# Kernel optimization log

Measured on AMD Instinct MI355X. Metric: run time of the kernel, lower is better.

Reference implementation:

```python
import jax, jax.numpy as jnp
import numpy as np


def _lstm_layer(x, Wih, Whh, bih, bhh):
    """Single-layer LSTM, batch_first, zero init state. PyTorch gate order i,f,g,o.
    x: [B,T,F]; Wih: [4H,F]; Whh: [4H,H]; bih,bhh: [4H]. Returns (outputs [B,T,H], h_T [B,H])."""
    B = x.shape[0]
    H = Whh.shape[1]
    # Precompute input projection for all timesteps (one big GEMM).
    pre = jnp.einsum('btf,gf->btg', x, Wih) + (bih + bhh)  # [B,T,4H]
    pre = jnp.swapaxes(pre, 0, 1)  # time-major [T,B,4H]

    def step(carry, p):
        h, c = carry
        gates = p + h @ Whh.T  # [B,4H]
        i, f, g, o = jnp.split(gates, 4, axis=-1)
        i = jax.nn.sigmoid(i)
        f = jax.nn.sigmoid(f)
        g = jnp.tanh(g)
        o = jax.nn.sigmoid(o)
        c = f * c + i * g
        h = o * jnp.tanh(c)
        return (h, c), h

    h0 = jnp.zeros((B, H), x.dtype)
    (hT, cT), hs = jax.lax.scan(step, (h0, h0), pre)
    return jnp.swapaxes(hs, 0, 1), hT


def setup_inputs() -> dict:
    key = jax.random.key(0)
    ks = jax.random.split(key, 20)
    B, T, F = 4096, 200, 36
    H1, H2, H3 = 16, 32, 16
    NC = 6

    def u(k, shape, h):
        s = 1.0 / np.sqrt(h)
        return jax.random.uniform(k, shape, jnp.float32, -s, s)

    inp = {
        'x': jax.random.normal(ks[0], (B, T, F), jnp.float32),
        'Wih1': u(ks[1], (4 * H1, F), H1), 'Whh1': u(ks[2], (4 * H1, H1), H1),
        'bih1': u(ks[3], (4 * H1,), H1), 'bhh1': u(ks[4], (4 * H1,), H1),
        'Wih2': u(ks[5], (4 * H2, H1), H2), 'Whh2': u(ks[6], (4 * H2, H2), H2),
        'bih2': u(ks[7], (4 * H2,), H2), 'bhh2': u(ks[8], (4 * H2,), H2),
        'Wih3': u(ks[9], (4 * H3, H2), H3), 'Whh3': u(ks[10], (4 * H3, H3), H3),
        'bih3': u(ks[11], (4 * H3,), H3), 'bhh3': u(ks[12], (4 * H3,), H3),
        'W_fc1': u(ks[13], (128, H3), H3), 'b_fc1': u(ks[14], (128,), H3),
        'W_fc2': u(ks[15], (32, 128), 128), 'b_fc2': u(ks[16], (32,), 128),
        'W_cls': u(ks[17], (NC, 32), 32), 'b_cls': u(ks[18], (NC,), 32),
    }
    return inp


def reference(x, Wih1, Whh1, bih1, bhh1, Wih2, Whh2, bih2, bhh2,
              Wih3, Whh3, bih3, bhh3, W_fc1, b_fc1, W_fc2, b_fc2, W_cls, b_cls):
    out1, _ = _lstm_layer(x, Wih1, Whh1, bih1, bhh1)
    out2, _ = _lstm_layer(out1, Wih2, Whh2, bih2, bhh2)
    _, hn = _lstm_layer(out2, Wih3, Whh3, bih3, bhh3)  # final hidden state [B,16]
    out = hn @ W_fc1.T + b_fc1
    out = out @ W_fc2.T + b_fc2
    out = out @ W_cls.T + b_cls
    return out
```

## Files before the change

kernel.cpp:

```cpp
#include <hip/hip_runtime.h>

typedef _Float16 hv8 __attribute__((ext_vector_type(8)));
typedef float    fv4 __attribute__((ext_vector_type(4)));
typedef unsigned int u32;

#define DEVI __device__ __forceinline__

static constexpr int T_   = 200;
static constexpr int ROWS = 8;
static constexpr int WS   = 72;
static constexpr int BTOT = 4096;

static constexpr int F1o = 0;
static constexpr int F2o = 1024;
static constexpr int XAo = 3072;
static constexpr int XBo = 3584;
static constexpr int F3o = 4096;
static constexpr int F_TOTAL = 4608;

#if __has_builtin(__builtin_amdgcn_rcpf)
DEVI float frcp(float x) { return __builtin_amdgcn_rcpf(x); }
#else
DEVI float frcp(float x) { return 1.0f / x; }
#endif
DEVI float fsig(float x)  { return frcp(1.0f + __expf(-x)); }
DEVI float ftanh(float x) { float e = __expf(2.0f * x); return 1.0f - 2.0f * frcp(e + 1.0f); }

DEVI u32 pk2h(float a, float b) {
    union { _Float16 h[2]; u32 u; } cv;
    cv.h[0] = (_Float16)a; cv.h[1] = (_Float16)b;
    return cv.u;
}

union HU { hv8 h; u32 u[4]; };

__global__ __launch_bounds__(256, 2) void lstm_fused(
    const float* __restrict__ xg,
    const float* __restrict__ Wih1, const float* __restrict__ Whh1,
    const float* __restrict__ bih1, const float* __restrict__ bhh1,
    const float* __restrict__ Wih2, const float* __restrict__ Whh2,
    const float* __restrict__ bih2, const float* __restrict__ bhh2,
    const float* __restrict__ Wih3, const float* __restrict__ Whh3,
    const float* __restrict__ bih3, const float* __restrict__ bhh3,
    const float* __restrict__ W_fc1, const float* __restrict__ b_fc1,
    const float* __restrict__ W_fc2, const float* __restrict__ b_fc2,
    const float* __restrict__ W_cls, const float* __restrict__ b_cls,
    float* __restrict__ outp)
{
    __shared__ __align__(16) _Float16 poolH[256 * WS];
    __shared__ float T2s[512];
    __shared__ float t2vs[32];
    __shared__ float Msh[96];
    __shared__ float vsh[6];

    const int tid  = threadIdx.x;
    const int wid  = tid >> 6;
    const int lane = tid & 63;
    const int nl   = lane & 15;
    const int quad = lane >> 4;
    const int b0   = blockIdx.x * ROWS;

    for (int idx = tid; idx < 256 * WS; idx += 256) {
        int n = idx / WS, k = idx - n * WS;
        int w = n >> 6, r = n & 63;
        int g = r >> 4, u = r & 15;
        float v = 0.f;
        if (w == 0) {
            int row = g * 16 + u;
            if (k < 36)       v = Wih1[row * 36 + k];
            else if (k == 36) v = bih1[row] + bhh1[row];
            else if (k >= 48 && k < 64) v = Whh1[row * 16 + (k - 48)];
        } else if (w <= 2) {
            int row = g * 32 + (w - 1) * 16 + u;
            if (k < 16)       v = Wih2[row * 16 + k];
            else if (k < 48)  {
                int kk = k - 16;
                int uu = (w == 1) ? kk : ((kk < 16) ? kk + 16 : kk - 16);
                v = Whh2[row * 32 + uu];
            }
            else if (k == 48) v = bih2[row] + bhh2[row];
        } else {
            int row = g * 16 + u;
            if (k < 32)       v = Wih3[row * 32 + k];
            else if (k < 48)  v = Whh3[row * 16 + (k - 32)];
            else if (k == 48) v = bih3[row] + bhh3[row];
        }
        poolH[idx] = (_Float16)v;
    }
    for (int idx = tid; idx < 512; idx += 256) {
        int b = idx >> 4, u = idx & 15;
        float acc = 0.f;
        for (int a = 0; a < 128; ++a) acc += W_fc2[b * 128 + a] * W_fc1[a * 16 + u];
        T2s[idx] = acc;
    }
    if (tid < 32) {
        float acc = b_fc2[tid];
        for (int a = 0; a < 128; ++a) acc += W_fc2[tid * 128 + a] * b_fc1[a];
        t2vs[tid] = acc;
    }
    __syncthreads();

    hv8 Wf[2][4];
    #pragma unroll
    for (int kt = 0; kt < 2; ++kt)
        #pragma unroll
        for (int mt = 0; mt < 4; ++mt)
            Wf[kt][mt] = *(const hv8*)&poolH[(wid * 64 + mt * 16 + nl) * WS + kt * 32 + quad * 8];
    if (tid < 96) {
        int u = tid / 6, j = tid - (tid / 6) * 6;
        float acc = 0.f;
        for (int b = 0; b < 32; ++b) acc += W_cls[j * 32 + b] * T2s[b * 16 + u];
        Msh[u * 6 + j] = acc;
    }
    if (tid < 6) {
        float acc = b_cls[tid];
        for (int b = 0; b < 32; ++b) acc += W_cls[tid * 32 + b] * t2vs[b];
        vsh[tid] = acc;
    }
    __syncthreads();

    for (int idx = tid; idx < F_TOTAL; idx += 256) poolH[idx] = (_Float16)0.f;

    fv4 xc[2][3], xn[2][3];
    const float* xb = xg;
    if (wid == 0) {
        int xr = b0 + nl; if (xr > BTOT - 1) xr = BTOT - 1;
        xb = xg + (size_t)xr * T_ * 36;
        #pragma unroll
        for (int g = 0; g < 2; ++g) {
            xn[g][0] = *(const fv4*)(xb + g * 36 + quad * 8);
            xn[g][1] = *(const fv4*)(xb + g * 36 + quad * 8 + 4);
            xn[g][2] = *(const fv4*)(xb + g * 36 + 32);
        }
    }
    __syncthreads();

    u32 pk01 = 0, pk23 = 0;
    float c_st[4] = {0.f, 0.f, 0.f, 0.f};
    const int s1x4 = ((quad & 1) * 32 + nl) * 4;
    const int s2x4 = s1x4 + 64;
    const u32 BIAS1 = 0x00003C00u;

    const int NI = T_ / 2 + 2;
    for (int s = 0; s < NI; ++s) {
        const int pp = (s - 1) & 1, wp = s & 1;
        bool act;
        if (wid == 0)      act = (s < T_ / 2);
        else if (wid <= 2) act = (s >= 1 && s <= T_ / 2);
        else               act = (s >= 2);

        HU pf0, pf1, pfx;
        if (act) {
            if (wid == 0) {
                #pragma unroll
                for (int g = 0; g < 2; ++g) { xc[g][0]=xn[g][0]; xc[g][1]=xn[g][1]; xc[g][2]=xn[g][2]; }
                #pragma unroll
                for (int g = 0; g < 2; ++g) {
                    int t = 2 * s + 2 + g;
                    if (t < T_) {
                        xn[g][0] = *(const fv4*)(xb + t * 36 + quad * 8);
                        xn[g][1] = *(const fv4*)(xb + t * 36 + quad * 8 + 4);
                        xn[g][2] = *(const fv4*)(xb + t * 36 + 32);
                    }
                }
            } else if (wid <= 2) {
                pf0.h = *(const hv8*)&poolH[F1o + ((pp * 2 + 0) * 16 + nl) * 16 + (quad & 1) * 8];
                pf1.h = *(const hv8*)&poolH[F1o + ((pp * 2 + 1) * 16 + nl) * 16 + (quad & 1) * 8];
                const int sibX = (wid == 1) ? XBo : XAo;
                pfx.h = *(const hv8*)&poolH[sibX + (1 * 16 + nl) * 16 + (quad & 1) * 8];
            } else {
                pf0.h = *(const hv8*)&poolH[F2o + ((pp * 2 + 0) * 16 + nl) * 32 + quad * 8];
                pf1.h = *(const hv8*)&poolH[F2o + ((pp * 2 + 1) * 16 + nl) * 32 + quad * 8];
            }

            HU x2g1;
            #pragma unroll
            for (int g = 0; g < 2; ++g) {
                u32 sA = (u32)__builtin_amdgcn_ds_bpermute(s1x4, (int)pk01);
                u32 sB = (u32)__builtin_amdgcn_ds_bpermute(s1x4, (int)pk23);
                u32 sC = (u32)__builtin_amdgcn_ds_bpermute(s2x4, (int)pk01);
                u32 sD = (u32)__builtin_amdgcn_ds_bpermute(s2x4, (int)pk23);

                HU bk0, bk1;
                if (wid == 0) {
                    bk0.u[0] = pk2h(xc[g][0][0], xc[g][0][1]);
                    bk0.u[1] = pk2h(xc[g][0][2], xc[g][0][3]);
                    bk0.u[2] = pk2h(xc[g][1][0], xc[g][1][1]);
                    bk0.u[3] = pk2h(xc[g][1][2], xc[g][1][3]);
                    if (quad >= 2) { bk1.u[0]=sA; bk1.u[1]=sB; bk1.u[2]=sC; bk1.u[3]=sD; }
                    else {
                        bk1.u[0] = pk2h(xc[g][2][0], xc[g][2][1]);
                        bk1.u[1] = pk2h(xc[g][2][2], xc[g][2][3]);
                        bk1.u[2] = BIAS1; bk1.u[3] = 0u;
                    }
                } else if (wid <= 2) {
                    if (quad < 2) bk0 = g ? pf1 : pf0;
                    else { bk0.u[0]=sA; bk0.u[1]=sB; bk0.u[2]=sC; bk0.u[3]=sD; }
                    if (quad < 2) bk1 = g ? x2g1 : pfx;
                    else { bk1.u[0]=BIAS1; bk1.u[1]=0u; bk1.u[2]=0u; bk1.u[3]=0u; }
                } else {
                    bk0 = g ? pf1 : pf0;
                    if (quad < 2) { bk1.u[0]=sA; bk1.u[1]=sB; bk1.u[2]=sC; bk1.u[3]=sD; }
                    else { bk1.u[0]=BIAS1; bk1.u[1]=0u; bk1.u[2]=0u; bk1.u[3]=0u; }
                }

                fv4 C[4] = {(fv4){0,0,0,0}, (fv4){0,0,0,0}, (fv4){0,0,0,0}, (fv4){0,0,0,0}};
                #pragma unroll
                for (int mt = 0; mt < 4; ++mt) C[mt] = __builtin_amdgcn_mfma_f32_16x16x32_f16(Wf[0][mt], bk0.h, C[mt], 0, 0, 0);
                #pragma unroll
                for (int mt = 0; mt < 4; ++mt) C[mt] = __builtin_amdgcn_mfma_f32_16x16x32_f16(Wf[1][mt], bk1.h, C[mt], 0, 0, 0);

                float h4[4];
                #pragma unroll
                for (int r = 0; r < 4; ++r) {
                    float gi = fsig(C[0][r]);
                    float gf = fsig(C[1][r]);
                    float gg = ftanh(C[2][r]);
                    float go = fsig(C[3][r]);
                    float c  = gf * c_st[r] + gi * gg;
                    c_st[r] = c;
                    h4[r] = go * ftanh(c);
                }
                pk01 = pk2h(h4[0], h4[1]);
                pk23 = pk2h(h4[2], h4[3]);

                if (wid == 0) {
                    u32* f1 = (u32*)&poolH[F1o + ((wp * 2 + g) * 16 + nl) * 16 + quad * 4];
                    f1[0] = pk01; f1[1] = pk23;
                } else if (wid <= 2) {
                    const int ownX = (wid == 1) ? XAo : XBo;
                    u32* xo = (u32*)&poolH[ownX + (g * 16 + nl) * 16 + quad * 4];
                    xo[0] = pk01; xo[1] = pk23;
                    const int ub = (wid == 1) ? 0 : 16;
                    u32* f2 = (u32*)&poolH[F2o + ((wp * 2 + g) * 16 + nl) * 32 + ub + quad * 4];
                    f2[0] = pk01; f2[1] = pk23;
                    if (g == 0) {
                        const int sibX = (wid == 1) ? XBo : XAo;
                        x2g1.h = *(const hv8*)&poolH[sibX + (0 * 16 + nl) * 16 + (quad & 1) * 8];
                    }
                } else {
                    u32* f3 = (u32*)&poolH[F3o + (g * 16 + nl) * 16 + quad * 4];
                    f3[0] = pk01; f3[1] = pk23;
                }
            }
        }
        __syncthreads();
    }

    if (tid < ROWS * 6) {
        int row = tid / 6, j = tid - (tid / 6) * 6;
        float acc = vsh[j];
        const int hb = F3o + 16 * 16 + row * 16;
        #pragma unroll
        for (int u = 0; u < 16; ++u)
            acc += (float)poolH[hb + u] * Msh[u * 6 + j];
        outp[(b0 + row) * 6 + j] = acc;
    }
}

extern "C" void kernel_launch(void* const* d_in, const int* in_sizes, int n_in,
                              void* d_out, int out_size, void* d_ws, size_t ws_size,
                              hipStream_t stream) {
    const float* x     = (const float*)d_in[0];
    const float* Wih1  = (const float*)d_in[1];
    const float* Whh1  = (const float*)d_in[2];
    const float* bih1  = (const float*)d_in[3];
    const float* bhh1  = (const float*)d_in[4];
    const float* Wih2  = (const float*)d_in[5];
    const float* Whh2  = (const float*)d_in[6];
    const float* bih2  = (const float*)d_in[7];
    const float* bhh2  = (const float*)d_in[8];
    const float* Wih3  = (const float*)d_in[9];
    const float* Whh3  = (const float*)d_in[10];
    const float* bih3  = (const float*)d_in[11];
    const float* bhh3  = (const float*)d_in[12];
    const float* W_fc1 = (const float*)d_in[13];
    const float* b_fc1 = (const float*)d_in[14];
    const float* W_fc2 = (const float*)d_in[15];
    const float* b_fc2 = (const float*)d_in[16];
    const float* W_cls = (const float*)d_in[17];
    const float* b_cls = (const float*)d_in[18];

    lstm_fused<<<512, 256, 0, stream>>>(x,
        Wih1, Whh1, bih1, bhh1,
        Wih2, Whh2, bih2, bhh2,
        Wih3, Whh3, bih3, bhh3,
        W_fc1, b_fc1, W_fc2, b_fc2, W_cls, b_cls,
        (float*)d_out);
}
```

Baseline: 435.9 us.

## Split recurrent MFMA from input projection to shorten per-step dependency chain

Reorganises the weight layout so each wave keeps separate input-projection and recurrent weight fragments. The input-side MFMAs for both sub-steps of an iteration are issued up front, off the recurrent critical path, and only one recurrent MFMA per gate tile remains serialised behind the bpermute of the previous hidden state. It also prefetches x two iterations ahead and replaces __syncthreads with a raw waitcnt+s_barrier. This costs extra MFMAs for layer 1 and more weight registers, and the hand-written barrier depends on LDS ordering being correct.

```diff
diff --git a/kernel.cpp b/kernel.cpp
--- a/kernel.cpp
+++ b/kernel.cpp
@@ -8,7 +8,7 @@
 
 static constexpr int T_   = 200;
 static constexpr int ROWS = 8;
-static constexpr int WS   = 72;
+static constexpr int WS   = 104;
 static constexpr int BTOT = 4096;
 
 static constexpr int F1o = 0;
@@ -69,21 +69,21 @@
             int row = g * 16 + u;
             if (k < 36)       v = Wih1[row * 36 + k];
             else if (k == 36) v = bih1[row] + bhh1[row];
-            else if (k >= 48 && k < 64) v = Whh1[row * 16 + (k - 48)];
+            else if (k >= 64 && k < 80) v = Whh1[row * 16 + (k - 64)];
         } else if (w <= 2) {
             int row = g * 32 + (w - 1) * 16 + u;
             if (k < 16)       v = Wih2[row * 16 + k];
-            else if (k < 48)  {
-                int kk = k - 16;
+            else if (k == 16) v = bih2[row] + bhh2[row];
+            else if (k >= 64 && k < 96) {
+                int kk = k - 64;
                 int uu = (w == 1) ? kk : ((kk < 16) ? kk + 16 : kk - 16);
                 v = Whh2[row * 32 + uu];
             }
-            else if (k == 48) v = bih2[row] + bhh2[row];
         } else {
             int row = g * 16 + u;
             if (k < 32)       v = Wih3[row * 32 + k];
-            else if (k < 48)  v = Whh3[row * 16 + (k - 32)];
-            else if (k == 48) v = bih3[row] + bhh3[row];
+            else if (k >= 64 && k < 80) v = Whh3[row * 16 + (k - 64)];
+            else if (k == 80) v = bih3[row] + bhh3[row];
         }
         poolH[idx] = (_Float16)v;
     }
@@ -100,12 +100,18 @@
     }
     __syncthreads();
 
-    hv8 Wf[2][4];
+    hv8 WI0[4], WI1[4], WH[4];
     #pragma unroll
-    for (int kt = 0; kt < 2; ++kt)
+    for (int mt = 0; mt < 4; ++mt) {
+        const int base = (wid * 64 + mt * 16 + nl) * WS;
+        WI0[mt] = *(const hv8*)&poolH[base + quad * 8];
+        WH[mt]  = *(const hv8*)&poolH[base + 64 + quad * 8];
+    }
+    if (wid == 0) {
         #pragma unroll
         for (int mt = 0; mt < 4; ++mt)
-            Wf[kt][mt] = *(const hv8*)&poolH[(wid * 64 + mt * 16 + nl) * WS + kt * 32 + quad * 8];
+            WI1[mt] = *(const hv8*)&poolH[(mt * 16 + nl) * WS + 32 + quad * 8];
+    }
     if (tid < 96) {
         int u = tid / 6, j = tid - (tid / 6) * 6;
         float acc = 0.f;
@@ -128,9 +134,12 @@
         xb = xg + (size_t)xr * T_ * 36;
         #pragma unroll
         for (int g = 0; g < 2; ++g) {
-            xn[g][0] = *(const fv4*)(xb + g * 36 + quad * 8);
-            xn[g][1] = *(const fv4*)(xb + g * 36 + quad * 8 + 4);
-            xn[g][2] = *(const fv4*)(xb + g * 36 + 32);
+            xc[g][0] = *(const fv4*)(xb + g * 36 + quad * 8);
+            xc[g][1] = *(const fv4*)(xb + g * 36 + quad * 8 + 4);
+            xc[g][2] = *(const fv4*)(xb + g * 36 + 32);
+            xn[g][0] = *(const fv4*)(xb + (2 + g) * 36 + quad * 8);
+            xn[g][1] = *(const fv4*)(xb + (2 + g) * 36 + quad * 8 + 4);
+            xn[g][2] = *(const fv4*)(xb + (2 + g) * 36 + 32);
         }
     }
     __syncthreads();
@@ -140,6 +149,54 @@
     const int s1x4 = ((quad & 1) * 32 + nl) * 4;
     const int s2x4 = s1x4 + 64;
     const u32 BIAS1 = 0x00003C00u;
+    const fv4 Z4 = (fv4){0.f, 0.f, 0.f, 0.f};
+
+#define DO_STEP(CARR, G)                                                              \
+    {                                                                                 \
+        u32 sA = (u32)__builtin_amdgcn_ds_bpermute(s1x4, (int)pk01);                  \
+        u32 sB = (u32)__builtin_amdgcn_ds_bpermute(s1x4, (int)pk23);                  \
+        u32 sC = (u32)__builtin_amdgcn_ds_bpermute(s2x4, (int)pk01);                  \
+        u32 sD = (u32)__builtin_amdgcn_ds_bpermute(s2x4, (int)pk23);                  \
+        HU bh;                                                                        \
+        if (quad < 2) { bh.u[0]=sA; bh.u[1]=sB; bh.u[2]=sC; bh.u[3]=sD; }             \
+        else if (wid == 0) { bh.u[0]=0u; bh.u[1]=0u; bh.u[2]=0u; bh.u[3]=0u; }        \
+        else if (wid <= 2) { bh = (G) ? x2g1 : pfx; }                                 \
+        else { bh.u[0]=(quad==2)?BIAS1:0u; bh.u[1]=0u; bh.u[2]=0u; bh.u[3]=0u; }      \
+        _Pragma("unroll")                                                             \
+        for (int mt = 0; mt < 4; ++mt)                                                \
+            CARR[mt] = __builtin_amdgcn_mfma_f32_16x16x32_f16(WH[mt], bh.h, CARR[mt], 0, 0, 0); \
+        float h4[4];                                                                  \
+        _Pragma("unroll")                                                             \
+        for (int r = 0; r < 4; ++r) {                                                 \
+            float gi = fsig(CARR[0][r]);                                              \
+            float gf = fsig(CARR[1][r]);                                              \
+            float gg = ftanh(CARR[2][r]);                                             \
+            float go = fsig(CARR[3][r]);                                              \
+            float c  = gf * c_st[r] + gi * gg;                                        \
+            c_st[r] = c;                                                              \
+            h4[r] = go * ftanh(c);                                                    \
+        }                                                                             \
+        pk01 = pk2h(h4[0], h4[1]);                                                    \
+        pk23 = pk2h(h4[2], h4[3]);                                                    \
+        if (wid == 0) {                                                               \
+            u32* f1 = (u32*)&poolH[F1o + ((wp * 2 + (G)) * 16 + nl) * 16 + quad * 4]; \
+            f1[0] = pk01; f1[1] = pk23;                                               \
+        } else if (wid <= 2) {                                                        \
+            const int ownX = (wid == 1) ? XAo : XBo;                                  \
+            u32* xo = (u32*)&poolH[ownX + ((G) * 16 + nl) * 16 + quad * 4];           \
+            xo[0] = pk01; xo[1] = pk23;                                               \
+            const int ub = (wid == 1) ? 0 : 16;                                       \
+            u32* f2 = (u32*)&poolH[F2o + ((wp * 2 + (G)) * 16 + nl) * 32 + ub + quad * 4]; \
+            f2[0] = pk01; f2[1] = pk23;                                               \
+            if ((G) == 0) {                                                           \
+                const int sibX = (wid == 1) ? XBo : XAo;                              \
+                x2g1.h = *(const hv8*)&poolH[sibX + (0 * 16 + nl) * 16 + (quad & 1) * 8]; \
+            }                                                                         \
+        } else {                                                                      \
+            u32* f3 = (u32*)&poolH[F3o + ((G) * 16 + nl) * 16 + quad * 4];            \
+            f3[0] = pk01; f3[1] = pk23;                                               \
+        }                                                                             \
+    }
 
     const int NI = T_ / 2 + 2;
     for (int s = 0; s < NI; ++s) {
@@ -149,14 +206,36 @@
         else if (wid <= 2) act = (s >= 1 && s <= T_ / 2);
         else               act = (s >= 2);
 
-        HU pf0, pf1, pfx;
         if (act) {
+            fv4 C0[4] = {Z4, Z4, Z4, Z4};
+            fv4 C1[4] = {Z4, Z4, Z4, Z4};
+            HU pfx, x2g1;
+
             if (wid == 0) {
                 #pragma unroll
+                for (int g = 0; g < 2; ++g) {
+                    HU bx0, bx1;
+                    bx0.u[0] = pk2h(xc[g][0][0], xc[g][0][1]);
+                    bx0.u[1] = pk2h(xc[g][0][2], xc[g][0][3]);
+                    bx0.u[2] = pk2h(xc[g][1][0], xc[g][1][1]);
+                    bx0.u[3] = pk2h(xc[g][1][2], xc[g][1][3]);
+                    if (quad == 0) {
+                        bx1.u[0] = pk2h(xc[g][2][0], xc[g][2][1]);
+                        bx1.u[1] = pk2h(xc[g][2][2], xc[g][2][3]);
+                        bx1.u[2] = BIAS1; bx1.u[3] = 0u;
+                    } else { bx1.u[0]=0u; bx1.u[1]=0u; bx1.u[2]=0u; bx1.u[3]=0u; }
+                    #pragma unroll
+                    for (int mt = 0; mt < 4; ++mt) {
+                        fv4* Cg = g ? C1 : C0;
+                        Cg[mt] = __builtin_amdgcn_mfma_f32_16x16x32_f16(WI0[mt], bx0.h, Cg[mt], 0, 0, 0);
+                        Cg[mt] = __builtin_amdgcn_mfma_f32_16x16x32_f16(WI1[mt], bx1.h, Cg[mt], 0, 0, 0);
+                    }
+                }
+                #pragma unroll
                 for (int g = 0; g < 2; ++g) { xc[g][0]=xn[g][0]; xc[g][1]=xn[g][1]; xc[g][2]=xn[g][2]; }
                 #pragma unroll
                 for (int g = 0; g < 2; ++g) {
-                    int t = 2 * s + 2 + g;
+                    int t = 2 * s + 4 + g;
                     if (t < T_) {
                         xn[g][0] = *(const fv4*)(xb + t * 36 + quad * 8);
                         xn[g][1] = *(const fv4*)(xb + t * 36 + quad * 8 + 4);
@@ -164,87 +243,37 @@
                     }
                 }
             } else if (wid <= 2) {
+                HU pf0, pf1;
                 pf0.h = *(const hv8*)&poolH[F1o + ((pp * 2 + 0) * 16 + nl) * 16 + (quad & 1) * 8];
                 pf1.h = *(const hv8*)&poolH[F1o + ((pp * 2 + 1) * 16 + nl) * 16 + (quad & 1) * 8];
-                const int sibX = (wid == 1) ? XBo : XAo;
-                pfx.h = *(const hv8*)&poolH[sibX + (1 * 16 + nl) * 16 + (quad & 1) * 8];
+                {
+                    const int sibX = (wid == 1) ? XBo : XAo;
+                    pfx.h = *(const hv8*)&poolH[sibX + (1 * 16 + nl) * 16 + (quad & 1) * 8];
+                }
+                HU b0, b1;
+                if (quad < 2)      { b0 = pf0; b1 = pf1; }
+                else if (quad == 2){ b0.u[0]=BIAS1; b0.u[1]=0u; b0.u[2]=0u; b0.u[3]=0u; b1 = b0; }
+                else               { b0.u[0]=0u; b0.u[1]=0u; b0.u[2]=0u; b0.u[3]=0u; b1 = b0; }
+                #pragma unroll
+                for (int mt = 0; mt < 4; ++mt) {
+                    C0[mt] = __builtin_amdgcn_mfma_f32_16x16x32_f16(WI0[mt], b0.h, C0[mt], 0, 0, 0);
+                    C1[mt] = __builtin_amdgcn_mfma_f32_16x16x32_f16(WI0[mt], b1.h, C1[mt], 0, 0, 0);
+                }
             } else {
-                pf0.h = *(const hv8*)&poolH[F2o + ((pp * 2 + 0) * 16 + nl) * 32 + quad * 8];
-                pf1.h = *(const hv8*)&poolH[F2o + ((pp * 2 + 1) * 16 + nl) * 32 + quad * 8];
+                HU b0, b1;
+                b0.h = *(const hv8*)&poolH[F2o + ((pp * 2 + 0) * 16 + nl) * 32 + quad * 8];
+                b1.h = *(const hv8*)&poolH[F2o + ((pp * 2 + 1) * 16 + nl) * 32 + quad * 8];
+                #pragma unroll
+                for (int mt = 0; mt < 4; ++mt) {
+                    C0[mt] = __builtin_amdgcn_mfma_f32_16x16x32_f16(WI0[mt], b0.h, C0[mt], 0, 0, 0);
+                    C1[mt] = __builtin_amdgcn_mfma_f32_16x16x32_f16(WI0[mt], b1.h, C1[mt], 0, 0, 0);
+                }
             }
 
-            HU x2g1;
-            #pragma unroll
-            for (int g = 0; g < 2; ++g) {
-                u32 sA = (u32)__builtin_amdgcn_ds_bpermute(s1x4, (int)pk01);
-                u32 sB = (u32)__builtin_amdgcn_ds_bpermute(s1x4, (int)pk23);
-                u32 sC = (u32)__builtin_amdgcn_ds_bpermute(s2x4, (int)pk01);
-                u32 sD = (u32)__builtin_amdgcn_ds_bpermute(s2x4, (int)pk23);
-
-                HU bk0, bk1;
-                if (wid == 0) {
-                    bk0.u[0] = pk2h(xc[g][0][0], xc[g][0][1]);
-                    bk0.u[1] = pk2h(xc[g][0][2], xc[g][0][3]);
-                    bk0.u[2] = pk2h(xc[g][1][0], xc[g][1][1]);
-                    bk0.u[3] = pk2h(xc[g][1][2], xc[g][1][3]);
-                    if (quad >= 2) { bk1.u[0]=sA; bk1.u[1]=sB; bk1.u[2]=sC; bk1.u[3]=sD; }
-                    else {
-                        bk1.u[0] = pk2h(xc[g][2][0], xc[g][2][1]);
-                        bk1.u[1] = pk2h(xc[g][2][2], xc[g][2][3]);
-                        bk1.u[2] = BIAS1; bk1.u[3] = 0u;
-                    }
-                } else if (wid <= 2) {
-                    if (quad < 2) bk0 = g ? pf1 : pf0;
-                    else { bk0.u[0]=sA; bk0.u[1]=sB; bk0.u[2]=sC; bk0.u[3]=sD; }
-                    if (quad < 2) bk1 = g ? x2g1 : pfx;
-                    else { bk1.u[0]=BIAS1; bk1.u[1]=0u; bk1.u[2]=0u; bk1.u[3]=0u; }
-                } else {
-                    bk0 = g ? pf1 : pf0;
-                    if (quad < 2) { bk1.u[0]=sA; bk1.u[1]=sB; bk1.u[2]=sC; bk1.u[3]=sD; }
-                    else { bk1.u[0]=BIAS1; bk1.u[1]=0u; bk1.u[2]=0u; bk1.u[3]=0u; }
-                }
-
-                fv4 C[4] = {(fv4){0,0,0,0}, (fv4){0,0,0,0}, (fv4){0,0,0,0}, (fv4){0,0,0,0}};
-                #pragma unroll
-                for (int mt = 0; mt < 4; ++mt) C[mt] = __builtin_amdgcn_mfma_f32_16x16x32_f16(Wf[0][mt], bk0.h, C[mt], 0, 0, 0);
-                #pragma unroll
-                for (int mt = 0; mt < 4; ++mt) C[mt] = __builtin_amdgcn_mfma_f32_16x16x32_f16(Wf[1][mt], bk1.h, C[mt], 0, 0, 0);
-
-                float h4[4];
-                #pragma unroll
-                for (int r = 0; r < 4; ++r) {
-                    float gi = fsig(C[0][r]);
-                    float gf = fsig(C[1][r]);
-                    float gg = ftanh(C[2][r]);
-                    float go = fsig(C[3][r]);
-                    float c  = gf * c_st[r] + gi * gg;
-                    c_st[r] = c;
-                    h4[r] = go * ftanh(c);
-                }
-                pk01 = pk2h(h4[0], h4[1]);
-                pk23 = pk2h(h4[2], h4[3]);
-
-                if (wid == 0) {
-                    u32* f1 = (u32*)&poolH[F1o + ((wp * 2 + g) * 16 + nl) * 16 + quad * 4];
-                    f1[0] = pk01; f1[1] = pk23;
-                } else if (wid <= 2) {
-                    const int ownX = (wid == 1) ? XAo : XBo;
-                    u32* xo = (u32*)&poolH[ownX + (g * 16 + nl) * 16 + quad * 4];
-                    xo[0] = pk01; xo[1] = pk23;
-                    const int ub = (wid == 1) ? 0 : 16;
-                    u32* f2 = (u32*)&poolH[F2o + ((wp * 2 + g) * 16 + nl) * 32 + ub + quad * 4];
-                    f2[0] = pk01; f2[1] = pk23;
-                    if (g == 0) {
-                        const int sibX = (wid == 1) ? XBo : XAo;
-                        x2g1.h = *(const hv8*)&poolH[sibX + (0 * 16 + nl) * 16 + (quad & 1) * 8];
-                    }
-                } else {
-                    u32* f3 = (u32*)&poolH[F3o + (g * 16 + nl) * 16 + quad * 4];
-                    f3[0] = pk01; f3[1] = pk23;
-                }
-            }
+            DO_STEP(C0, 0)
+            DO_STEP(C1, 1)
         }
-        __syncthreads();
+        asm volatile("s_waitcnt lgkmcnt(0)\n\ts_barrier" ::: "memory");
     }
 
     if (tid < ROWS * 6) {
@@ -256,6 +285,7 @@
             acc += (float)poolH[hb + u] * Msh[u * 6 + j];
         outp[(b0 + row) * 6 + j] = acc;
     }
+#undef DO_STEP
 }
 
 extern "C" void kernel_launch(void* const* d_in, const int* in_sizes, int n_in,
```

Result: slower. 449.3 us (+3.1%).

## Split LSTM cell activations across lanes using DPP rotate to halve transcendental work

Applied to the files above, without the earlier changes.

Only 8 batch rows are real per block, but all 16 MFMA columns ran the full gate nonlinearities. Each lane now processes two of the four accumulator rows. Lanes in the upper half take rows 2-3 from the lower half through a DPP row-rotate, so the sigmoid and tanh work per lane is halved. The h packing, bpermute indices and shared-memory store layout are rewritten to match the new lane-to-element mapping. In exchange it adds DPP moves and selects, and needs the index mapping to be correct.

```diff
diff --git a/kernel.cpp b/kernel.cpp
--- a/kernel.cpp
+++ b/kernel.cpp
@@ -17,6 +17,7 @@
 static constexpr int XBo = 3584;
 static constexpr int F3o = 4096;
 static constexpr int F_TOTAL = 4608;
+static constexpr int F1u = F1o / 2, F2u = F2o / 2, XAu = XAo / 2, XBu = XBo / 2, F3u = F3o / 2;
 
 #if __has_builtin(__builtin_amdgcn_rcpf)
 DEVI float frcp(float x) { return __builtin_amdgcn_rcpf(x); }
@@ -30,6 +31,12 @@
     union { _Float16 h[2]; u32 u; } cv;
     cv.h[0] = (_Float16)a; cv.h[1] = (_Float16)b;
     return cv.u;
+}
+
+DEVI float ror8(float x) {
+    union { float f; int i; } cv; cv.f = x;
+    cv.i = __builtin_amdgcn_mov_dpp(cv.i, 0x128, 0xf, 0xf, true);
+    return cv.f;
 }
 
 union HU { hv8 h; u32 u[4]; };
@@ -124,7 +131,8 @@
     fv4 xc[2][3], xn[2][3];
     const float* xb = xg;
     if (wid == 0) {
-        int xr = b0 + nl; if (xr > BTOT - 1) xr = BTOT - 1;
+        int xr = b0 + (nl < ROWS ? nl : ROWS - 1);
+        if (xr > BTOT - 1) xr = BTOT - 1;
         xb = xg + (size_t)xr * T_ * 36;
         #pragma unroll
         for (int g = 0; g < 2; ++g) {
@@ -135,10 +143,14 @@
     }
     __syncthreads();
 
-    u32 pk01 = 0, pk23 = 0;
-    float c_st[4] = {0.f, 0.f, 0.f, 0.f};
-    const int s1x4 = ((quad & 1) * 32 + nl) * 4;
-    const int s2x4 = s1x4 + 64;
+    u32 pkAB = 0;
+    float c_st[2] = {0.f, 0.f};
+    const bool loRole = (nl < 8);
+    const int  nlb = nl & 7, ro = nl >> 3;
+    const int iA = ((quad & 1) * 32 + nlb) * 4;
+    const int iB = iA + 32;
+    const int iC = iA + 64;
+    const int iD = iA + 96;
     const u32 BIAS1 = 0x00003C00u;
 
     const int NI = T_ / 2 + 2;
@@ -176,10 +188,10 @@
             HU x2g1;
             #pragma unroll
             for (int g = 0; g < 2; ++g) {
-                u32 sA = (u32)__builtin_amdgcn_ds_bpermute(s1x4, (int)pk01);
-                u32 sB = (u32)__builtin_amdgcn_ds_bpermute(s1x4, (int)pk23);
-                u32 sC = (u32)__builtin_amdgcn_ds_bpermute(s2x4, (int)pk01);
-                u32 sD = (u32)__builtin_amdgcn_ds_bpermute(s2x4, (int)pk23);
+                u32 sA = (u32)__builtin_amdgcn_ds_bpermute(iA, (int)pkAB);
+                u32 sB = (u32)__builtin_amdgcn_ds_bpermute(iB, (int)pkAB);
+                u32 sC = (u32)__builtin_amdgcn_ds_bpermute(iC, (int)pkAB);
+                u32 sD = (u32)__builtin_amdgcn_ds_bpermute(iD, (int)pkAB);
 
                 HU bk0, bk1;
                 if (wid == 0) {
@@ -210,37 +222,39 @@
                 #pragma unroll
                 for (int mt = 0; mt < 4; ++mt) C[mt] = __builtin_amdgcn_mfma_f32_16x16x32_f16(Wf[1][mt], bk1.h, C[mt], 0, 0, 0);
 
-                float h4[4];
-                #pragma unroll
-                for (int r = 0; r < 4; ++r) {
-                    float gi = fsig(C[0][r]);
-                    float gf = fsig(C[1][r]);
-                    float gg = ftanh(C[2][r]);
-                    float go = fsig(C[3][r]);
-                    float c  = gf * c_st[r] + gi * gg;
-                    c_st[r] = c;
-                    h4[r] = go * ftanh(c);
-                }
-                pk01 = pk2h(h4[0], h4[1]);
-                pk23 = pk2h(h4[2], h4[3]);
-
+                float e0[4], e1[4];
+                #pragma unroll
+                for (int mt = 0; mt < 4; ++mt) {
+                    float t2 = ror8(C[mt][2]);
+                    float t3 = ror8(C[mt][3]);
+                    e0[mt] = loRole ? C[mt][0] : t2;
+                    e1[mt] = loRole ? C[mt][1] : t3;
+                }
+                float h0, h1;
+                {
+                    float gi = fsig(e0[0]), gf = fsig(e0[1]), gg = ftanh(e0[2]), go = fsig(e0[3]);
+                    float c = gf * c_st[0] + gi * gg; c_st[0] = c; h0 = go * ftanh(c);
+                }
+                {
+                    float gi = fsig(e1[0]), gf = fsig(e1[1]), gg = ftanh(e1[2]), go = fsig(e1[3]);
+                    float c = gf * c_st[1] + gi * gg; c_st[1] = c; h1 = go * ftanh(c);
+                }
+                pkAB = pk2h(h0, h1);
+
+                u32* pb = (u32*)poolH;
                 if (wid == 0) {
-                    u32* f1 = (u32*)&poolH[F1o + ((wp * 2 + g) * 16 + nl) * 16 + quad * 4];
-                    f1[0] = pk01; f1[1] = pk23;
+                    pb[F1u + ((wp * 2 + g) * 16 + nlb) * 8 + quad * 2 + ro] = pkAB;
                 } else if (wid <= 2) {
-                    const int ownX = (wid == 1) ? XAo : XBo;
-                    u32* xo = (u32*)&poolH[ownX + (g * 16 + nl) * 16 + quad * 4];
-                    xo[0] = pk01; xo[1] = pk23;
-                    const int ub = (wid == 1) ? 0 : 16;
-                    u32* f2 = (u32*)&poolH[F2o + ((wp * 2 + g) * 16 + nl) * 32 + ub + quad * 4];
-                    f2[0] = pk01; f2[1] = pk23;
+                    const int ownXu = (wid == 1) ? XAu : XBu;
+                    pb[ownXu + (g * 16 + nlb) * 8 + quad * 2 + ro] = pkAB;
+                    const int ub2 = (wid == 1) ? 0 : 8;
+                    pb[F2u + ((wp * 2 + g) * 16 + nlb) * 16 + ub2 + quad * 2 + ro] = pkAB;
                     if (g == 0) {
                         const int sibX = (wid == 1) ? XBo : XAo;
                         x2g1.h = *(const hv8*)&poolH[sibX + (0 * 16 + nl) * 16 + (quad & 1) * 8];
                     }
                 } else {
-                    u32* f3 = (u32*)&poolH[F3o + (g * 16 + nl) * 16 + quad * 4];
-                    f3[0] = pk01; f3[1] = pk23;
+                    pb[F3u + (g * 16 + nlb) * 8 + quad * 2 + ro] = pkAB;
                 }
             }
         }
```

Result: faster. 400.1 us (-8.2%).
